# Optimization experiments

Measured on AMD Instinct MI355X. Metric: run time of the kernel, lower is better.

The kernel has to match this reference:

```python
import jax, jax.numpy as jnp
import numpy as np
import math

D_MODEL = 256
SIGMA = 1.0


def _sinusoidal_pe(L, d_model, dtype=jnp.float32):
    # pe[l, 2i] = sin(l * w_i), pe[l, 2i+1] = cos(l * w_i)
    position = jnp.arange(L, dtype=dtype)[:, None]                       # [L,1]
    div_term = jnp.exp(jnp.arange(0, d_model, 2, dtype=dtype) * (-math.log(10000.0) / d_model))
    pe = jnp.zeros((L, d_model), dtype=dtype)
    pe = pe.at[:, 0::2].set(jnp.sin(position * div_term))
    pe = pe.at[:, 1::2].set(jnp.cos(position * div_term))
    return pe  # [L, d_model]


def setup_inputs() -> dict:
    key = jax.random.key(0)
    # scale 0.05 keeps pairwise sq-distances O(1) so S = exp(-d/2) is non-degenerate
    x = jax.random.normal(key, (4, 4096, 256), dtype=jnp.float32) * 0.05
    return {"x": x}


def reference(x):
    B, L, D = x.shape
    pe = _sinusoidal_pe(L, D_MODEL, dtype=x.dtype)[None]                 # [1,L,D]
    # pairwise squared distances via the expansion ||a||^2+||b||^2-2ab (avoids [B,L,L,D])
    sq = jnp.sum(x * x, axis=-1)                                         # [B,L]
    gram = jnp.einsum('bld,bmd->blm', x, x)                              # [B,L,L]
    dist_sq = jnp.maximum(sq[:, :, None] + sq[:, None, :] - 2.0 * gram, 0.0)
    S = jnp.exp(-dist_sq / (2.0 * SIGMA ** 2))                           # [B,L,L]
    sem = jnp.einsum('blm,bmd->bld', S, x) / jnp.sum(S, axis=-1, keepdims=True)
    return x + pe + sem
```

## Files before the change

### kernel.cpp

```cpp
#include <hip/hip_runtime.h>

typedef unsigned char u8;
typedef float f32x4 __attribute__((ext_vector_type(4)));
typedef float f32x16 __attribute__((ext_vector_type(16)));
typedef int i32x8 __attribute__((ext_vector_type(8)));

#define LL 4096
#define PSTR 144
#define SCALE 16.0f
#define GSCALE (1.0f/256.0f)
#define FREQC (-0.03597789207803197f)
#define ONE_SC 0x7F7F7F7F

__device__ __forceinline__ i32x8 PK16(uint4 a, uint4 b) {
  i32x8 r;
  r[0] = (int)a.x; r[1] = (int)a.y; r[2] = (int)a.z; r[3] = (int)a.w;
  r[4] = (int)b.x; r[5] = (int)b.y; r[6] = (int)b.z; r[7] = (int)b.w;
  return r;
}

typedef __attribute__((address_space(3))) u8 lds_u8;
typedef __attribute__((address_space(1))) u8 glb_u8;
__device__ __forceinline__ void dma16(const u8* g, u8* l) {
  __builtin_amdgcn_global_load_lds((const glb_u8*)g, (lds_u8*)l, 16, 0, 0);
}

__global__ __launch_bounds__(512) void prep3(const float* __restrict__ x, u8* __restrict__ xbf,
                                             u8* __restrict__ xT, float* __restrict__ sq) {
  __shared__ u8 T2[256 * 80];
  const int blk = blockIdx.x;
  const int b = blk >> 6, ch = blk & 63;
  const int j0 = ch << 6;
  const int tid = threadIdx.x;
  const int wv = tid >> 6, ln = tid & 63;
  const long bL = (long)b * LL;
  const float4* x4 = (const float4*)x + (bL + j0) * 64;
  unsigned* xb4 = (unsigned*)xbf + (bL + j0) * 64;

  #pragma unroll
  for (int g = 0; g < 2; ++g) {
    int pkw[4];
    #pragma unroll
    for (int ii = 0; ii < 4; ++ii) {
      const int row = 8 * wv + 4 * g + ii;
      float4 v = x4[row * 64 + ln];
      float s = v.x * v.x + v.y * v.y + v.z * v.z + v.w * v.w;
      #pragma unroll
      for (int o = 32; o; o >>= 1) s += __shfl_xor(s, o);
      if (ln == 0) sq[bL + j0 + row] = s;
      int pk = __builtin_amdgcn_cvt_pk_fp8_f32(v.x * SCALE, v.y * SCALE, 0, false);
      pk = __builtin_amdgcn_cvt_pk_fp8_f32(v.z * SCALE, v.w * SCALE, pk, true);
      const int sdw = ((((ln >> 2) ^ ((j0 + row) & 15)) << 2)) | (ln & 3);
      xb4[row * 64 + sdw] = (unsigned)pk;
      pkw[ii] = pk;
    }
    const int rb = 8 * wv + 4 * g;
    #pragma unroll
    for (int k = 0; k < 4; ++k) {
      const unsigned sel = (unsigned)(k | ((4 + k) << 8));
      unsigned m01 = __builtin_amdgcn_perm((unsigned)pkw[1], (unsigned)pkw[0], sel);
      unsigned m23 = __builtin_amdgcn_perm((unsigned)pkw[3], (unsigned)pkw[2], sel);
      unsigned tw  = __builtin_amdgcn_perm(m23, m01, 0x05040100u);
      *(unsigned*)(T2 + (4 * ln + k) * 80 + rb) = tw;
    }
  }
  __syncthreads();
  #pragma unroll
  for (int db = 0; db < 2; ++db) {
    const int d = db * 128 + (tid >> 2);
    const int cl = tid & 3;
    const int c16 = ((ch & 1) << 2) | cl;
    const int p = c16 ^ (d & 7);
    uint4 ov = *(const uint4*)(T2 + d * 80 + 16 * cl);
    *(uint4*)(xT + (((long)(b << 8) + d) << 12) + ((ch >> 1) << 7) + (p << 4)) = ov;
  }
}

__global__ __launch_bounds__(512, 2) void tpe_main(
    const u8* __restrict__ xbf, const u8* __restrict__ xT,
    const float* __restrict__ sqv,
    const float* __restrict__ x, float* __restrict__ out) {
  __shared__ __align__(16) u8 Kt[2][32768];
  __shared__ __align__(16) u8 Ps[2][64 * PSTR];
  __shared__ float lred[8][64];
  __shared__ float linv[64];

  const int tid = threadIdx.x;
  const int w = tid >> 6;
  const int lane = tid & 63;
  const int l15 = lane & 15, l31 = lane & 31;
  const int q4 = lane >> 4;
  const int q2 = lane >> 5;

  const int blk = blockIdx.x;
  const int b = (blk & 7) >> 1;
  const int qt = ((blk >> 3) << 1) | (blk & 1);
  const int q0 = qt << 6;
  const long bL = (long)b * LL;

  i32x8 qmx[4][2];
  float qa[4];
  #pragma unroll
  for (int t = 0; t < 4; ++t) {
    const int row = q0 + 16 * t + l15;
    const u8* qrow = xbf + ((bL + row) << 8);
    #pragma unroll
    for (int u = 0; u < 2; ++u) {
      const int cb = 8 * u + 2 * q4;
      uint4 lo = *(const uint4*)(qrow + (((cb + 0) ^ l15) << 4));
      uint4 hi = *(const uint4*)(qrow + (((cb + 1) ^ l15) << 4));
      qmx[t][u] = PK16(lo, hi);
    }
    qa[t] = -0.5f * sqv[bL + row];
  }

  f32x16 oacc[2];
  #pragma unroll
  for (int rb = 0; rb < 2; ++rb)
    #pragma unroll
    for (int k = 0; k < 16; ++k) oacc[rb][k] = 0.f;
  float rsacc[4] = {0.f, 0.f, 0.f, 0.f};

  const u8* kbat = xbf + (bL << 8);
  const u8* vseg = xT + (((long)(b << 8) + 32 * w + l31) << 12);
  const int vk7 = l31 & 7;

  i32x8 vfA[2], vfB[2];

  #pragma unroll
  for (int c = 0; c < 4; ++c) {
    int off = c * 8192 + tid * 16;
    dma16(kbat + off, Kt[0] + off);
  }
  __syncthreads();

#define TPE_ITER(IT, KCUR, KNXT, PPREV, PCUR, VFC, VFN)                                     \
  {                                                                                         \
    const int j0 = (IT) << 7;                                                               \
    if ((IT) < 31) {    \
      const u8* ks = kbat + ((long)((IT) + 1) << 15);                                       \
      _Pragma("unroll")                                                                     \
      for (int c = 0; c < 4; ++c) {                                                         \
        int off = c * 8192 + tid * 16;                                                      \
        dma16(ks + off, (KNXT) + off);                                                      \
      }                                                                                     \
    }                                                                                       \
    float4 skv4 = *(const float4*)(sqv + bL + j0 + 16 * w + 4 * q4);                        \
    if ((IT) != 0) {  \
      _Pragma("unroll")                                                                     \
      for (int u = 0; u < 2; ++u) {                                                         \
        const u8* pr0 = (PPREV) + l31 * PSTR + 64 * u + 32 * q2;                            \
        i32x8 pa0 = PK16(*(const uint4*)(pr0), *(const uint4*)(pr0 + 16));                  \
        i32x8 pa1 = PK16(*(const uint4*)(pr0 + 32 * PSTR),                                  \
                         *(const uint4*)(pr0 + 32 * PSTR + 16));                            \
        oacc[0] = __builtin_amdgcn_mfma_scale_f32_32x32x64_f8f6f4(                          \
            pa0, VFC[u], oacc[0], 0, 0, 0, ONE_SC, 0, ONE_SC);                              \
        oacc[1] = __builtin_amdgcn_mfma_scale_f32_32x32x64_f8f6f4(                          \
            pa1, VFC[u], oacc[1], 0, 0, 0, ONE_SC, 0, ONE_SC);                              \
      }                                                                                     \
    }                                                                                       \
    _Pragma("unroll")              \
    for (int u = 0; u < 2; ++u) {                                                           \
      const int cb = 4 * u + 2 * q2;                                                        \
      uint4 v0 = *(const uint4*)(vseg + j0 + (((cb + 0) ^ vk7) << 4));                      \
      uint4 v1 = *(const uint4*)(vseg + j0 + (((cb + 1) ^ vk7) << 4));                      \
      VFN[u] = PK16(v0, v1);                                                                \
    }                                                                                       \
    {                            \
      const int krow = 16 * w + l15;                                                        \
      const u8* kb2 = (KCUR) + krow * 256;                                                  \
      f32x4 sacc[4];                                                                        \
      _Pragma("unroll")                                                                     \
      for (int t = 0; t < 4; ++t) {                                                         \
        sacc[t][0] = 0.f; sacc[t][1] = 0.f; sacc[t][2] = 0.f; sacc[t][3] = 0.f;             \
      }                                                                                     \
      _Pragma("unroll")                                                                     \
      for (int u = 0; u < 2; ++u) {                                                         \
        const int cb = 8 * u + 2 * q4;                                                      \
        uint4 klo = *(const uint4*)(kb2 + (((cb + 0) ^ l15) << 4));                         \
        uint4 khi = *(const uint4*)(kb2 + (((cb + 1) ^ l15) << 4));                         \
        i32x8 af = PK16(klo, khi);                                                          \
        _Pragma("unroll")                                                                   \
        for (int t = 0; t < 4; ++t)                                                         \
          sacc[t] = __builtin_amdgcn_mfma_scale_f32_16x16x128_f8f6f4(                       \
              af, qmx[t][u], sacc[t], 0, 0, 0, ONE_SC, 0, ONE_SC);                          \
      }                                                                                     \
      _Pragma("unroll")        \
      for (int t = 0; t < 4; ++t) {                 \
        float p0 = __expf(fminf(fmaf(sacc[t][0], GSCALE, qa[t] + skv4.x), 0.f));            \
        float p1 = __expf(fminf(fmaf(sacc[t][1], GSCALE, qa[t] + skv4.y), 0.f));            \
        float p2 = __expf(fminf(fmaf(sacc[t][2], GSCALE, qa[t] + skv4.z), 0.f));            \
        float p3 = __expf(fminf(fmaf(sacc[t][3], GSCALE, qa[t] + skv4.w), 0.f));            \
        rsacc[t] += (p0 + p1) + (p2 + p3);                                                  \
        int pk = __builtin_amdgcn_cvt_pk_fp8_f32(p0, p1, 0, false);                         \
        pk = __builtin_amdgcn_cvt_pk_fp8_f32(p2, p3, pk, true);                             \
        *(int*)((PCUR) + (16 * t + l15) * PSTR + 16 * w + 4 * q4) = pk;                     \
      }                                                                                     \
    }                                                                                       \
    __syncthreads();         \
  }

  for (int it2 = 0; it2 < 16; ++it2) {
    TPE_ITER(2 * it2,     Kt[0], Kt[1], Ps[1], Ps[0], vfA, vfB)
    TPE_ITER(2 * it2 + 1, Kt[1], Kt[0], Ps[0], Ps[1], vfB, vfA)
  }
#undef TPE_ITER

  #pragma unroll
  for (int u = 0; u < 2; ++u) {
    const u8* pr0 = Ps[1] + l31 * PSTR + 64 * u + 32 * q2;
    i32x8 pa0 = PK16(*(const uint4*)(pr0), *(const uint4*)(pr0 + 16));
    i32x8 pa1 = PK16(*(const uint4*)(pr0 + 32 * PSTR), *(const uint4*)(pr0 + 32 * PSTR + 16));
    oacc[0] = __builtin_amdgcn_mfma_scale_f32_32x32x64_f8f6f4(
        pa0, vfA[u], oacc[0], 0, 0, 0, ONE_SC, 0, ONE_SC);
    oacc[1] = __builtin_amdgcn_mfma_scale_f32_32x32x64_f8f6f4(
        pa1, vfA[u], oacc[1], 0, 0, 0, ONE_SC, 0, ONE_SC);
  }

  #pragma unroll
  for (int t = 0; t < 4; ++t) {
    float r = rsacc[t];
    r += __shfl_xor(r, 16);
    r += __shfl_xor(r, 32);
    if (lane < 16) lred[w][16 * t + l15] = r;
  }
  __syncthreads();
  if (tid < 64) {
    float s = 0.f;
    #pragma unroll
    for (int ww = 0; ww < 8; ++ww) s += lred[ww][tid];
    linv[tid] = 0.0625f / s;
  }
  __syncthreads();
  const int col = 32 * w + l31;
  const float freq = __expf((float)(col & ~1) * FREQC);
  #pragma unroll
  for (int rb = 0; rb < 2; ++rb) {
    #pragma unroll
    for (int reg = 0; reg < 16; ++reg) {
      int row = 32 * rb + 4 * q2 + (reg & 3) + 8 * (reg >> 2);
      int l = q0 + row;
      float ang = (float)l * freq;
      float pv = (col & 1) ? __cosf(ang) : __sinf(ang);
      long off = ((bL + l) << 8) + col;
      out[off] = oacc[rb][reg] * linv[row] + x[off] + pv;
    }
  }
}

extern "C" void kernel_launch(void* const* d_in, const int* in_sizes, int n_in,
                              void* d_out, int out_size, void* d_ws, size_t ws_size,
                              hipStream_t stream) {
  const float* x = (const float*)d_in[0];
  float* out = (float*)d_out;
  char* ws = (char*)d_ws;
  u8* xbf = (u8*)ws;
  u8* xT = (u8*)(ws + 4194304);
  float* sq = (float*)(ws + 8388608);
  prep3<<<256, 512, 0, stream>>>(x, xbf, xT, sq);
  tpe_main<<<256, 512, 0, stream>>>(xbf, xT, sq, x, out);
}
```

Measured before the change: 123.9 us.

## Split waves into producer (QK+exp) and consumer (PV) groups with 1024 threads

Doubles the block to 16 waves and specialises them: eight waves compute the QK scores, exponentials and fp8 P tile, while the other eight load V fragments and run the PV MFMAs on the previous tile. MFMA sections are bracketed with s_setprio to favour matrix issue. The aim is to overlap the exp/convert work with the PV matrix work across wave groups instead of serialising it within each wave. In exchange, launch bounds drop to one block per CU, and the V fragment is no longer double-buffered in registers.

Measured after the change: 247.8 us. 2x slower.

```diff
diff --git a/kernel.cpp b/kernel.cpp
--- a/kernel.cpp
+++ b/kernel.cpp
@@ -76,7 +76,7 @@
   }
 }
 
-__global__ __launch_bounds__(512, 2) void tpe_main(
+__global__ __launch_bounds__(1024, 1) void tpe_main(
     const u8* __restrict__ xbf, const u8* __restrict__ xT,
     const float* __restrict__ sqv,
     const float* __restrict__ x, float* __restrict__ out) {
@@ -91,6 +91,8 @@
   const int l15 = lane & 15, l31 = lane & 31;
   const int q4 = lane >> 4;
   const int q2 = lane >> 5;
+  const bool prod = (w < 8);
+  const int wp = w & 7;
 
   const int blk = blockIdx.x;
   const int b = (blk & 7) >> 1;
@@ -98,82 +100,87 @@
   const int q0 = qt << 6;
   const long bL = (long)b * LL;
 
+  const u8* kbat = xbf + (bL << 8);
+
   i32x8 qmx[4][2];
   float qa[4];
+  float rsacc[4] = {0.f, 0.f, 0.f, 0.f};
+  f32x16 oacc[2];
+  i32x8 vf[2];
+  const u8* vseg = xT + (((long)(b << 8) + 32 * wp + l31) << 12);
+  const int vk7 = l31 & 7;
+
+  if (prod) {
+    #pragma unroll
+    for (int t = 0; t < 4; ++t) {
+      const int row = q0 + 16 * t + l15;
+      const u8* qrow = xbf + ((bL + row) << 8);
+      #pragma unroll
+      for (int u = 0; u < 2; ++u) {
+        const int cb = 8 * u + 2 * q4;
+        uint4 lo = *(const uint4*)(qrow + (((cb + 0) ^ l15) << 4));
+        uint4 hi = *(const uint4*)(qrow + (((cb + 1) ^ l15) << 4));
+        qmx[t][u] = PK16(lo, hi);
+      }
+      qa[t] = -0.5f * sqv[bL + row];
+    }
+  } else {
+    #pragma unroll
+    for (int rb = 0; rb < 2; ++rb)
+      #pragma unroll
+      for (int k = 0; k < 16; ++k) oacc[rb][k] = 0.f;
+  }
+
   #pragma unroll
-  for (int t = 0; t < 4; ++t) {
-    const int row = q0 + 16 * t + l15;
-    const u8* qrow = xbf + ((bL + row) << 8);
-    #pragma unroll
-    for (int u = 0; u < 2; ++u) {
-      const int cb = 8 * u + 2 * q4;
-      uint4 lo = *(const uint4*)(qrow + (((cb + 0) ^ l15) << 4));
-      uint4 hi = *(const uint4*)(qrow + (((cb + 1) ^ l15) << 4));
-      qmx[t][u] = PK16(lo, hi);
-    }
-    qa[t] = -0.5f * sqv[bL + row];
-  }
-
-  f32x16 oacc[2];
-  #pragma unroll
-  for (int rb = 0; rb < 2; ++rb)
-    #pragma unroll
-    for (int k = 0; k < 16; ++k) oacc[rb][k] = 0.f;
-  float rsacc[4] = {0.f, 0.f, 0.f, 0.f};
-
-  const u8* kbat = xbf + (bL << 8);
-  const u8* vseg = xT + (((long)(b << 8) + 32 * w + l31) << 12);
-  const int vk7 = l31 & 7;
-
-  i32x8 vfA[2], vfB[2];
-
-  #pragma unroll
-  for (int c = 0; c < 4; ++c) {
-    int off = c * 8192 + tid * 16;
+  for (int c = 0; c < 2; ++c) {
+    int off = c * 16384 + tid * 16;
     dma16(kbat + off, Kt[0] + off);
   }
   __syncthreads();
 
-#define TPE_ITER(IT, KCUR, KNXT, PPREV, PCUR, VFC, VFN)                                     \
+#define TPE_ITER(IT, KCUR, KNXT, PPREV, PCUR)                                               \
   {                                                                                         \
     const int j0 = (IT) << 7;                                                               \
     if ((IT) < 31) {    \
       const u8* ks = kbat + ((long)((IT) + 1) << 15);                                       \
       _Pragma("unroll")                                                                     \
-      for (int c = 0; c < 4; ++c) {                                                         \
-        int off = c * 8192 + tid * 16;                                                      \
+      for (int c = 0; c < 2; ++c) {                                                         \
+        int off = c * 16384 + tid * 16;                                                     \
         dma16(ks + off, (KNXT) + off);                                                      \
       }                                                                                     \
     }                                                                                       \
-    float4 skv4 = *(const float4*)(sqv + bL + j0 + 16 * w + 4 * q4);                        \
-    if ((IT) != 0) {  \
-      _Pragma("unroll")                                                                     \
+    if (!prod) {       \
+      if ((IT) != 0) {                                                                      \
+        __builtin_amdgcn_s_setprio(1);                                                      \
+        _Pragma("unroll")                                                                   \
+        for (int u = 0; u < 2; ++u) {                                                       \
+          const u8* pr0 = (PPREV) + l31 * PSTR + 64 * u + 32 * q2;                          \
+          i32x8 pa0 = PK16(*(const uint4*)(pr0), *(const uint4*)(pr0 + 16));                \
+          i32x8 pa1 = PK16(*(const uint4*)(pr0 + 32 * PSTR),                                \
+                           *(const uint4*)(pr0 + 32 * PSTR + 16));                          \
+          oacc[0] = __builtin_amdgcn_mfma_scale_f32_32x32x64_f8f6f4(                        \
+              pa0, vf[u], oacc[0], 0, 0, 0, ONE_SC, 0, ONE_SC);                             \
+          oacc[1] = __builtin_amdgcn_mfma_scale_f32_32x32x64_f8f6f4(                        \
+              pa1, vf[u], oacc[1], 0, 0, 0, ONE_SC, 0, ONE_SC);                             \
+        }                                                                                   \
+        __builtin_amdgcn_s_setprio(0);                                                      \
+      }                                                                                     \
+      _Pragma("unroll")  \
       for (int u = 0; u < 2; ++u) {                                                         \
-        const u8* pr0 = (PPREV) + l31 * PSTR + 64 * u + 32 * q2;                            \
-        i32x8 pa0 = PK16(*(const uint4*)(pr0), *(const uint4*)(pr0 + 16));                  \
-        i32x8 pa1 = PK16(*(const uint4*)(pr0 + 32 * PSTR),                                  \
-                         *(const uint4*)(pr0 + 32 * PSTR + 16));                            \
-        oacc[0] = __builtin_amdgcn_mfma_scale_f32_32x32x64_f8f6f4(                          \
-            pa0, VFC[u], oacc[0], 0, 0, 0, ONE_SC, 0, ONE_SC);                              \
-        oacc[1] = __builtin_amdgcn_mfma_scale_f32_32x32x64_f8f6f4(                          \
-            pa1, VFC[u], oacc[1], 0, 0, 0, ONE_SC, 0, ONE_SC);                              \
-      }                                                                                     \
-    }                                                                                       \
-    _Pragma("unroll")              \
-    for (int u = 0; u < 2; ++u) {                                                           \
-      const int cb = 4 * u + 2 * q2;                                                        \
-      uint4 v0 = *(const uint4*)(vseg + j0 + (((cb + 0) ^ vk7) << 4));                      \
-      uint4 v1 = *(const uint4*)(vseg + j0 + (((cb + 1) ^ vk7) << 4));                      \
-      VFN[u] = PK16(v0, v1);                                                                \
-    }                                                                                       \
-    {                            \
-      const int krow = 16 * w + l15;                                                        \
-      const u8* kb2 = (KCUR) + krow * 256;                                                  \
+        const int cb = 4 * u + 2 * q2;                                                      \
+        uint4 v0 = *(const uint4*)(vseg + j0 + (((cb + 0) ^ vk7) << 4));                    \
+        uint4 v1 = *(const uint4*)(vseg + j0 + (((cb + 1) ^ vk7) << 4));                    \
+        vf[u] = PK16(v0, v1);                                                               \
+      }                                                                                     \
+    } else {                      \
+      float4 skv4 = *(const float4*)(sqv + bL + j0 + 16 * wp + 4 * q4);                     \
+      const u8* kb2 = (KCUR) + (16 * wp + l15) * 256;                                       \
       f32x4 sacc[4];                                                                        \
       _Pragma("unroll")                                                                     \
       for (int t = 0; t < 4; ++t) {                                                         \
         sacc[t][0] = 0.f; sacc[t][1] = 0.f; sacc[t][2] = 0.f; sacc[t][3] = 0.f;             \
       }                                                                                     \
+      __builtin_amdgcn_s_setprio(1);                                                        \
       _Pragma("unroll")                                                                     \
       for (int u = 0; u < 2; ++u) {                                                         \
         const int cb = 8 * u + 2 * q4;                                                      \
@@ -185,8 +192,9 @@
           sacc[t] = __builtin_amdgcn_mfma_scale_f32_16x16x128_f8f6f4(                       \
               af, qmx[t][u], sacc[t], 0, 0, 0, ONE_SC, 0, ONE_SC);                          \
       }                                                                                     \
+      __builtin_amdgcn_s_setprio(0);                                                        \
       _Pragma("unroll")        \
-      for (int t = 0; t < 4; ++t) {                 \
+      for (int t = 0; t < 4; ++t) {                \
         float p0 = __expf(fminf(fmaf(sacc[t][0], GSCALE, qa[t] + skv4.x), 0.f));            \
         float p1 = __expf(fminf(fmaf(sacc[t][1], GSCALE, qa[t] + skv4.y), 0.f));            \
         float p2 = __expf(fminf(fmaf(sacc[t][2], GSCALE, qa[t] + skv4.z), 0.f));            \
@@ -194,35 +202,39 @@
         rsacc[t] += (p0 + p1) + (p2 + p3);                                                  \
         int pk = __builtin_amdgcn_cvt_pk_fp8_f32(p0, p1, 0, false);                         \
         pk = __builtin_amdgcn_cvt_pk_fp8_f32(p2, p3, pk, true);                             \
-        *(int*)((PCUR) + (16 * t + l15) * PSTR + 16 * w + 4 * q4) = pk;                     \
+        *(int*)((PCUR) + (16 * t + l15) * PSTR + 16 * wp + 4 * q4) = pk;                    \
       }                                                                                     \
     }                                                                                       \
     __syncthreads();         \
   }
 
   for (int it2 = 0; it2 < 16; ++it2) {
-    TPE_ITER(2 * it2,     Kt[0], Kt[1], Ps[1], Ps[0], vfA, vfB)
-    TPE_ITER(2 * it2 + 1, Kt[1], Kt[0], Ps[0], Ps[1], vfB, vfA)
+    TPE_ITER(2 * it2,     Kt[0], Kt[1], Ps[1], Ps[0])
+    TPE_ITER(2 * it2 + 1, Kt[1], Kt[0], Ps[0], Ps[1])
   }
 #undef TPE_ITER
 
-  #pragma unroll
-  for (int u = 0; u < 2; ++u) {
-    const u8* pr0 = Ps[1] + l31 * PSTR + 64 * u + 32 * q2;
-    i32x8 pa0 = PK16(*(const uint4*)(pr0), *(const uint4*)(pr0 + 16));
-    i32x8 pa1 = PK16(*(const uint4*)(pr0 + 32 * PSTR), *(const uint4*)(pr0 + 32 * PSTR + 16));
-    oacc[0] = __builtin_amdgcn_mfma_scale_f32_32x32x64_f8f6f4(
-        pa0, vfA[u], oacc[0], 0, 0, 0, ONE_SC, 0, ONE_SC);
-    oacc[1] = __builtin_amdgcn_mfma_scale_f32_32x32x64_f8f6f4(
-        pa1, vfA[u], oacc[1], 0, 0, 0, ONE_SC, 0, ONE_SC);
-  }
-
-  #pragma unroll
-  for (int t = 0; t < 4; ++t) {
-    float r = rsacc[t];
-    r += __shfl_xor(r, 16);
-    r += __shfl_xor(r, 32);
-    if (lane < 16) lred[w][16 * t + l15] = r;
+  if (!prod) {
+    #pragma unroll
+    for (int u = 0; u < 2; ++u) {
+      const u8* pr0 = Ps[1] + l31 * PSTR + 64 * u + 32 * q2;
+      i32x8 pa0 = PK16(*(const uint4*)(pr0), *(const uint4*)(pr0 + 16));
+      i32x8 pa1 = PK16(*(const uint4*)(pr0 + 32 * PSTR), *(const uint4*)(pr0 + 32 * PSTR + 16));
+      oacc[0] = __builtin_amdgcn_mfma_scale_f32_32x32x64_f8f6f4(
+          pa0, vf[u], oacc[0], 0, 0, 0, ONE_SC, 0, ONE_SC);
+      oacc[1] = __builtin_amdgcn_mfma_scale_f32_32x32x64_f8f6f4(
+          pa1, vf[u], oacc[1], 0, 0, 0, ONE_SC, 0, ONE_SC);
+    }
+  }
+
+  if (prod) {
+    #pragma unroll
+    for (int t = 0; t < 4; ++t) {
+      float r = rsacc[t];
+      r += __shfl_xor(r, 16);
+      r += __shfl_xor(r, 32);
+      if (lane < 16) lred[wp][16 * t + l15] = r;
+    }
   }
   __syncthreads();
   if (tid < 64) {
@@ -232,18 +244,20 @@
     linv[tid] = 0.0625f / s;
   }
   __syncthreads();
-  const int col = 32 * w + l31;
-  const float freq = __expf((float)(col & ~1) * FREQC);
-  #pragma unroll
-  for (int rb = 0; rb < 2; ++rb) {
-    #pragma unroll
-    for (int reg = 0; reg < 16; ++reg) {
-      int row = 32 * rb + 4 * q2 + (reg & 3) + 8 * (reg >> 2);
-      int l = q0 + row;
-      float ang = (float)l * freq;
-      float pv = (col & 1) ? __cosf(ang) : __sinf(ang);
-      long off = ((bL + l) << 8) + col;
-      out[off] = oacc[rb][reg] * linv[row] + x[off] + pv;
+  if (!prod) {
+    const int col = 32 * wp + l31;
+    const float freq = __expf((float)(col & ~1) * FREQC);
+    #pragma unroll
+    for (int rb = 0; rb < 2; ++rb) {
+      #pragma unroll
+      for (int reg = 0; reg < 16; ++reg) {
+        int row = 32 * rb + 4 * q2 + (reg & 3) + 8 * (reg >> 2);
+        int l = q0 + row;
+        float ang = (float)l * freq;
+        float pv = (col & 1) ? __cosf(ang) : __sinf(ang);
+        long off = ((bL + l) << 8) + col;
+        out[off] = oacc[rb][reg] * linv[row] + x[off] + pv;
+      }
     }
   }
 }
@@ -258,5 +272,5 @@
   u8* xT = (u8*)(ws + 4194304);
   float* sq = (float*)(ws + 8388608);
   prep3<<<256, 512, 0, stream>>>(x, xbf, xT, sq);
-  tpe_main<<<256, 512, 0, stream>>>(xbf, xT, sq, x, out);
-}
+  tpe_main<<<256, 1024, 0, stream>>>(xbf, xT, sq, x, out);
+}
```
